# Performance work log

Hardware: AMD Instinct MI355X
Metric: run time of the kernel (lower is better)

## Reference

```python
import jax, jax.numpy as jnp
import numpy as np

E = 304   # embedding size
H = 304   # hidden size
D = 61    # dict_size
B = 256   # batch
T = 512   # frame_num
P = 68    # max_phn_num


def _gru_cell(h, x, Wih, Whh, bih, bhh):
    # PyTorch GRU cell: gates ordered (r, z, n)
    gi = x @ Wih.T + bih            # [B, 3H]
    gh = h @ Whh.T + bhh            # [B, 3H]
    i_r, i_z, i_n = jnp.split(gi, 3, axis=-1)
    h_r, h_z, h_n = jnp.split(gh, 3, axis=-1)
    r = jax.nn.sigmoid(i_r + h_r)
    z = jax.nn.sigmoid(i_z + h_z)
    n = jnp.tanh(i_n + r * h_n)
    return (1.0 - z) * n + z * h


def _run_gru(xs, h0, Wih, Whh, bih, bhh):
    # xs: [B, L, E] -> outputs [B, L, H], final hidden [B, H]
    def step(h, x):
        h = _gru_cell(h, x, Wih, Whh, bih, bhh)
        return h, h
    h_last, outs = jax.lax.scan(step, h0, jnp.swapaxes(xs, 0, 1))
    return jnp.swapaxes(outs, 0, 1), h_last


def setup_inputs() -> dict:
    key = jax.random.key(0)
    ks = jax.random.split(key, 12)
    s = 1.0 / np.sqrt(H)
    u = lambda k, shp: jax.random.uniform(k, shp, jnp.float32, -s, s)
    return {
        'input': jax.random.normal(ks[0], (B, T, E), jnp.float32),
        'target': jax.random.randint(ks[1], (B, P, 1), 0, D),
        'teacher_forcing': 1,
        'enc_Wih': u(ks[2], (3 * H, E)),
        'enc_Whh': u(ks[3], (3 * H, H)),
        'enc_bih': u(ks[4], (3 * H,)),
        'enc_bhh': u(ks[5], (3 * H,)),
        'emb': jax.random.normal(ks[6], (D, E), jnp.float32),
        'dec_Wih': u(ks[7], (3 * H, E)),
        'dec_Whh': u(ks[8], (3 * H, H)),
        'dec_bih': u(ks[9], (3 * H,)),
        'dec_bhh': u(ks[10], (3 * H,)),
        'lin_W': u(ks[11], (D, H)),
        'lin_b': jnp.zeros((D,), jnp.float32),
    }


def reference(input, target, teacher_forcing, enc_Wih, enc_Whh, enc_bih, enc_bhh,
              emb, dec_Wih, dec_Whh, dec_bih, dec_bhh, lin_W, lin_b):
    batch = input.shape[0]
    h0 = jnp.zeros((batch, H), input.dtype)
    # Encoder: the python loop over frames is mathematically a full GRU scan
    enc_outs, enc_h = _run_gru(input, h0, enc_Wih, enc_Whh, enc_bih, enc_bhh)
    # Decoder (teacher_forcing == 1): input tokens are [0, target[:,1], ..., target[:,P-1]]
    toks = jnp.concatenate(
        [jnp.zeros((batch, 1), target.dtype), target[:, 1:, 0]], axis=1)  # [B, P]
    dec_x = emb[toks]                                                      # [B, P, E]
    dec_outs, _ = _run_gru(dec_x, enc_h, dec_Wih, dec_Whh, dec_bih, dec_bhh)
    logits = dec_outs @ lin_W.T + lin_b        # [B, P, D]
    softmaxs = jax.nn.softmax(logits, axis=-1)
    softmax_cal = softmaxs[:, :-1, :].reshape(-1, D)
    target_cal = target[:, 1:, :].reshape(-1)
    asr_outputs = jnp.argmax(softmaxs[:, :-1, :], axis=2)[:, :, None]
    return softmax_cal, target_cal, asr_outputs
```

## Files before the change

### kernel.cpp

```cpp
#include <hip/hip_runtime.h>
#include <math.h>

#define B_   256
#define E_   304
#define H_   304
#define T_   512
#define P_   68
#define PD   67
#define D_   61
#define NCB  16
#define NBG  16
#define RB   16
#define CBH  19
#define GC   57
#define NSTEP (T_ + PD)
#define HW   152
#define BLK_ULL (RB * HW)
#define LROW 328
#define LROWU 164
#define NKS  10
#define RSTR 20
#define SC_LO 2048.0f
#define SC_INV 4.8828125e-4f

typedef unsigned long long ull;
typedef _Float16 half8 __attribute__((ext_vector_type(8)));
typedef _Float16 half2v __attribute__((ext_vector_type(2)));
typedef float f32x4 __attribute__((ext_vector_type(4)));

__global__ __launch_bounds__(256, 1) void gru_persist(
    const float* __restrict__ input,
    const int*   __restrict__ target,
    const float* __restrict__ emb,
    const float* __restrict__ eWih, const float* __restrict__ eWhh,
    const float* __restrict__ ebih, const float* __restrict__ ebhh,
    const float* __restrict__ dWih, const float* __restrict__ dWhh,
    const float* __restrict__ dbih, const float* __restrict__ dbhh,
    float* hbuf,
    float* __restrict__ dec_outs,
    int* flg)
{
    __shared__ _Float16 opH[2][RB * LROW];
    __shared__ _Float16 opL[2][RB * LROW];
    __shared__ float red0[64 * RSTR], red1[64 * RSTR];
    __shared__ float bi_l[2][GC], bh_l[2][GC];

    const int tid  = threadIdx.x;
    const int L    = blockIdx.x;
    const int xcd  = L & 7;
    const int yy   = L >> 3;
    const int cb   = yy & 15;
    const int bg   = ((yy >> 4) << 3) | xcd;
    const int r0   = bg * RB;
    const int c0h  = cb * CBH;
    const int wv   = tid >> 6;
    const int lane = tid & 63;

    half8 wih_h[NKS], wih_l[NKS], whh_h[NKS], whh_l[NKS];

    auto packw = [&](const float* W, half8* wh, half8* wl) {
        int c = wv * 16 + (lane & 15);
        bool valid = (c < GC);
        int g = valid ? c / CBH : 0, j19 = valid ? c - (c / CBH) * CBH : 0;
        const float* wp = W + (size_t)(g * H_ + c0h + j19) * 304;
        int grp = (lane >> 4) * 8;
        #pragma unroll
        for (int ks = 0; ks < NKS; ++ks) {
            half8 vh, vl;
            #pragma unroll
            for (int j = 0; j < 8; ++j) {
                int k = ks * 32 + grp + j;
                float v = (valid && k < 304) ? wp[k] : 0.f;
                _Float16 hi = (_Float16)v;
                float rres = v - (float)hi;
                vh[j] = hi;
                vl[j] = (_Float16)(rres * SC_LO);
            }
            wh[ks] = vh; wl[ks] = vl;
        }
    };

    auto gemm = [&](const _Float16* aH, const _Float16* aL,
                    const half8* wh, const half8* wl, float* red) {
        const int base = (lane & 15) * LROW + (lane >> 4) * 8;
        f32x4 a0 = {0.f, 0.f, 0.f, 0.f}, a1 = a0, a2 = a0;
        #pragma unroll
        for (int ks = 0; ks < NKS; ++ks) {
            half8 Ah = *(const half8*)&aH[base + ks * 32];
            half8 Al = *(const half8*)&aL[base + ks * 32];
            a0 = __builtin_amdgcn_mfma_f32_16x16x32_f16(Ah, wh[ks], a0, 0, 0, 0);
            a1 = __builtin_amdgcn_mfma_f32_16x16x32_f16(Ah, wl[ks], a1, 0, 0, 0);
            a2 = __builtin_amdgcn_mfma_f32_16x16x32_f16(Al, wh[ks], a2, 0, 0, 0);
        }
        f32x4 r = a0 + (a1 + a2) * SC_INV;
        int rb = (wv * 16 + (lane & 15)) * RSTR + (lane >> 4) * 4;
        *(f32x4*)&red[rb] = r;
    };

    auto cvtstore = [&](ull u, int plane, int idx) {
        float a0 = __uint_as_float((unsigned)u);
        float a1 = __uint_as_float((unsigned)(u >> 32));
        _Float16 h0 = (_Float16)a0, h1 = (_Float16)a1;
        float r0f = a0 - (float)h0, r1f = a1 - (float)h1;
        half2v vh; vh.x = h0; vh.y = h1;
        half2v vl; vl.x = (_Float16)(r0f * SC_LO); vl.y = (_Float16)(r1f * SC_LO);
        ((half2v*)&opH[plane][0])[idx] = vh;
        ((half2v*)&opL[plane][0])[idx] = vl;
    };

    packw(eWih, wih_h, wih_l);
    packw(eWhh, whh_h, whh_l);
    if (tid < GC) {
        int g = tid / CBH, j = tid - (tid / CBH) * CBH;
        bi_l[0][tid] = ebih[g * H_ + c0h + j];
        bh_l[0][tid] = ebhh[g * H_ + c0h + j];
        bi_l[1][tid] = dbih[g * H_ + c0h + j];
        bh_l[1][tid] = dbhh[g * H_ + c0h + j];
    }

    for (int f = tid; f < RB * LROW; f += 256) {
        ((unsigned*)opH)[f] = 0u;
        ((unsigned*)opL)[f] = 0u;
    }
    __syncthreads();
    {
        const ull* xin = (const ull*)input;
        #pragma unroll
        for (int i = 0; i < 10; ++i) {
            int f = tid + 256 * i;
            if (i < 9 || f < BLK_ULL) {
                int rr = f / HW, q = f - (f / HW) * HW;
                cvtstore(xin[(size_t)(r0 + rr) * T_ * HW + q], 0, rr * LROWU + q);
            }
        }
    }
    __syncthreads();
    gemm(opH[0], opL[0], wih_h, wih_l, red0);
    ull xr[10];
    {
        const ull* xin = (const ull*)input;
        #pragma unroll
        for (int i = 0; i < 10; ++i) {
            int f = tid + 256 * i;
            if (i < 9 || f < BLK_ULL) {
                int rr = f / HW, q = f - (f / HW) * HW;
                xr[i] = xin[((size_t)(r0 + rr) * T_ + 1) * HW + q];
            }
        }
    }

    for (int s = 0; s < NSTEP; ++s) {
        __syncthreads();
        const bool enc = (s < T_);
        if (s == T_) packw(dWhh, whh_h, whh_l);

        ull hreg[10];
        if (s > 0) {
            const ull* hsrc = (const ull*)(hbuf + (size_t)(s & 1) * (B_ * H_))
                              + (size_t)r0 * HW;
            #pragma unroll
            for (int i = 0; i < 10; ++i) {
                int f = tid + 256 * i;
                if (i < 9 || f < BLK_ULL)
                    hreg[i] = __hip_atomic_load(hsrc + f, __ATOMIC_RELAXED,
                                                __HIP_MEMORY_SCOPE_AGENT);
            }
        }
        if (s + 1 < NSTEP) {
            #pragma unroll
            for (int i = 0; i < 10; ++i) {
                int f = tid + 256 * i;
                if (i < 9 || f < BLK_ULL) {
                    int rr = f / HW, q = f - (f / HW) * HW;
                    cvtstore(xr[i], 0, rr * LROWU + q);
                }
            }
        }
        if (s > 0) {
            #pragma unroll
            for (int i = 0; i < 10; ++i) {
                int f = tid + 256 * i;
                if (i < 9 || f < BLK_ULL) {
                    int rr = f / HW, q = f - (f / HW) * HW;
                    cvtstore(hreg[i], 1, rr * LROWU + q);
                }
            }
        }
        if (s + 2 < NSTEP) {
            if (s + 2 < T_) {
                const ull* xin = (const ull*)input;
                #pragma unroll
                for (int i = 0; i < 10; ++i) {
                    int f = tid + 256 * i;
                    if (i < 9 || f < BLK_ULL) {
                        int rr = f / HW, q = f - (f / HW) * HW;
                        xr[i] = xin[((size_t)(r0 + rr) * T_ + (s + 2)) * HW + q];
                    }
                }
            } else {
                const ull* eb = (const ull*)emb;
                int p2 = s + 2 - T_;
                #pragma unroll
                for (int i = 0; i < 10; ++i) {
                    int f = tid + 256 * i;
                    if (i < 9 || f < BLK_ULL) {
                        int rr = f / HW, q = f - (f / HW) * HW;
                        int tok = (p2 == 0) ? 0 : target[(r0 + rr) * P_ + p2];
                        xr[i] = eb[(size_t)tok * HW + q];
                    }
                }
            }
        }
        __syncthreads();

        gemm(opH[1], opL[1], whh_h, whh_l, red1);
        __syncthreads();

        float* hdst = hbuf + (size_t)((s + 1) & 1) * (B_ * H_);
        for (int o = tid; o < RB * CBH; o += 256) {
            int rr = o / CBH, j = o - (o / CBH) * CBH;
            int col = c0h + j;
            int ph = enc ? 0 : 1;
            float Gi[3], Gh[3];
            #pragma unroll
            for (int g = 0; g < 3; ++g) {
                int c = g * CBH + j;
                Gi[g] = red0[c * RSTR + rr] + bi_l[ph][c];
                Gh[g] = red1[c * RSTR + rr] + bh_l[ph][c];
            }
            float rg = 1.f / (1.f + expf(-(Gi[0] + Gh[0])));
            float zg = 1.f / (1.f + expf(-(Gi[1] + Gh[1])));
            float ng = tanhf(Gi[2] + rg * Gh[2]);
            float hv = (float)opH[1][rr * LROW + col]
                     + (float)opL[1][rr * LROW + col] * SC_INV;
            float hnew = (1.f - zg) * ng + zg * hv;
            __hip_atomic_store(&hdst[(size_t)(r0 + rr) * H_ + col], hnew,
                               __ATOMIC_RELAXED, __HIP_MEMORY_SCOPE_AGENT);
            if (!enc)
                dec_outs[((size_t)(r0 + rr) * PD + (s - T_)) * H_ + col] = hnew;
        }
        __syncthreads();

        if (s + 1 < NSTEP) {
            if (tid == 0)
                __hip_atomic_store(flg + (bg * NCB + cb) * 16, s + 1,
                                   __ATOMIC_RELAXED, __HIP_MEMORY_SCOPE_AGENT);
            if (s + 1 == T_) packw(dWih, wih_h, wih_l);
            gemm(opH[0], opL[0], wih_h, wih_l, red0);
            if (wv == 0) {
                const int tgt = s + 1;
                const int* fp = flg + (bg * NCB + (lane & 15)) * 16;
                for (;;) {
                    int f = (lane < NCB)
                        ? __hip_atomic_load(fp, __ATOMIC_RELAXED,
                                            __HIP_MEMORY_SCOPE_AGENT)
                        : tgt;
                    if (__all(f >= tgt)) break;
                    __builtin_amdgcn_s_sleep(1);
                }
            }
        }
    }
}

__global__ __launch_bounds__(256) void logits_softmax(
    const float* __restrict__ dec_outs,
    const float* __restrict__ linW,
    const float* __restrict__ linb,
    const int* __restrict__ target,
    float* __restrict__ out)
{
    __shared__ float wsm[H_][64];
    __shared__ float rs[4][H_];
    const int tid = threadIdx.x;
    const int wv = tid >> 6, l = tid & 63;

    for (int f = tid; f < H_ * 64; f += 256) {
        int k = f >> 6, ll = f & 63;
        wsm[k][ll] = (ll < D_) ? linW[(size_t)ll * H_ + k] : 0.f;
    }
    const int r = blockIdx.x * 4 + wv;
    const float* rowp = dec_outs + (size_t)r * H_;
    for (int k = l; k < H_; k += 64) rs[wv][k] = rowp[k];
    __syncthreads();

    float acc = -1e30f;
    if (l < D_) {
        acc = linb[l];
        #pragma unroll 4
        for (int k = 0; k < H_; ++k) acc += rs[wv][k] * wsm[k][l];
    }
    float m = acc;
    for (int off = 32; off; off >>= 1) m = fmaxf(m, __shfl_xor(m, off));
    float e = (l < D_) ? expf(acc - m) : 0.f;
    float s = e;
    for (int off = 32; off; off >>= 1) s += __shfl_xor(s, off);
    float av = acc; int ai = l;
    for (int off = 32; off; off >>= 1) {
        float ov = __shfl_xor(av, off);
        int oi = __shfl_xor(ai, off);
        if (ov > av || (ov == av && oi < ai)) { av = ov; ai = oi; }
    }
    const int b = r / PD, p = r - (r / PD) * PD;
    const size_t OFF1 = (size_t)B_ * PD * D_;
    const size_t OFF2 = OFF1 + (size_t)B_ * PD;
    if (l < D_)        out[(size_t)r * D_ + l] = e / s;
    else if (l == D_)  out[OFF1 + r] = (float)target[b * P_ + p + 1];
    else if (l == D_ + 1) out[OFF2 + r] = (float)ai;
}

extern "C" void kernel_launch(void* const* d_in, const int* in_sizes, int n_in,
                              void* d_out, int out_size, void* d_ws, size_t ws_size,
                              hipStream_t stream)
{
    const float* input  = (const float*)d_in[0];
    const int*   target = (const int*)d_in[1];
    const float* eWih = (const float*)d_in[3];
    const float* eWhh = (const float*)d_in[4];
    const float* ebih = (const float*)d_in[5];
    const float* ebhh = (const float*)d_in[6];
    const float* emb  = (const float*)d_in[7];
    const float* dWih = (const float*)d_in[8];
    const float* dWhh = (const float*)d_in[9];
    const float* dbih = (const float*)d_in[10];
    const float* dbhh = (const float*)d_in[11];
    const float* linW = (const float*)d_in[12];
    const float* linb = (const float*)d_in[13];
    float* out = (float*)d_out;

    int*   flg      = (int*)d_ws;
    float* hbuf     = (float*)d_ws + NBG * NCB * 16;
    float* dec_outs = hbuf + 2 * (size_t)B_ * H_;

    (void)hipMemsetAsync(flg, 0, NBG * NCB * 16 * sizeof(int), stream);

    gru_persist<<<dim3(256), 256, 0, stream>>>(
        input, target, emb,
        eWih, eWhh, ebih, ebhh,
        dWih, dWhh, dbih, dbhh,
        hbuf, dec_outs, flg);

    logits_softmax<<<dim3(B_ * PD / 4), 256, 0, stream>>>(
        dec_outs, linW, linb, target, out);
}
```

Measured before the change: 2.390 ms.

## Move flag spin-wait to step start and triple-buffer x operand planes

Moves the cross-block flag wait from the end of each step, where only wave 0 waited, to the start of the next step right before the hidden-state loads. Every wave now polls, and the leading __syncthreads is removed. The x operand is double-buffered across two LDS planes with h in a third, so the next step's input GEMM can write without racing the current staging. The change also swaps expf/tanhf for fast exp and rcp versions, precomputes per-thread index arithmetic, and pads the flag stride to 32 ints. The risks are extra LDS use and slightly less accurate activations, and correctness now depends on every wave seeing the flags before it loads h.

After: 2.444 ms. +2.2%, slower.

```diff
diff --git a/kernel.cpp b/kernel.cpp
--- a/kernel.cpp
+++ b/kernel.cpp
@@ -20,6 +20,7 @@
 #define LROWU 164
 #define NKS  10
 #define RSTR 20
+#define FSTR 32
 #define SC_LO 2048.0f
 #define SC_INV 4.8828125e-4f
 
@@ -27,6 +28,15 @@
 typedef _Float16 half8 __attribute__((ext_vector_type(8)));
 typedef _Float16 half2v __attribute__((ext_vector_type(2)));
 typedef float f32x4 __attribute__((ext_vector_type(4)));
+
+__device__ __forceinline__ float fsigmoid(float x) {
+    float e = __expf(-x);
+    return __builtin_amdgcn_rcpf(1.f + e);
+}
+__device__ __forceinline__ float ftanh(float x) {
+    float e = __expf(2.f * x);
+    return 1.f - 2.f * __builtin_amdgcn_rcpf(1.f + e);
+}
 
 __global__ __launch_bounds__(256, 1) void gru_persist(
     const float* __restrict__ input,
@@ -40,8 +50,8 @@
     float* __restrict__ dec_outs,
     int* flg)
 {
-    __shared__ _Float16 opH[2][RB * LROW];
-    __shared__ _Float16 opL[2][RB * LROW];
+    __shared__ _Float16 opH[3][RB * LROW];
+    __shared__ _Float16 opL[3][RB * LROW];
     __shared__ float red0[64 * RSTR], red1[64 * RSTR];
     __shared__ float bi_l[2][GC], bh_l[2][GC];
 
@@ -57,6 +67,24 @@
     const int lane = tid & 63;
 
     half8 wih_h[NKS], wih_l[NKS], whh_h[NKS], whh_l[NKS];
+
+    int  idxA[10];
+    size_t xbA[10];
+    int  rrA[10], qA[10], tgA[10];
+    #pragma unroll
+    for (int i = 0; i < 10; ++i) {
+        int f = tid + 256 * i;
+        int rr = f / HW, q = f - (f / HW) * HW;
+        rrA[i] = rr; qA[i] = q;
+        idxA[i] = rr * LROWU + q;
+        xbA[i]  = (size_t)(r0 + rr) * T_ * HW + q;
+        tgA[i]  = (r0 + rr) * P_;
+    }
+    const bool gv0 = tid < RB * CBH;
+    const int  gr0 = tid / CBH, gj0 = tid - (tid / CBH) * CBH;
+    const bool gv1 = tid + 256 < RB * CBH;
+    const int  o1  = tid + 256;
+    const int  gr1 = o1 / CBH, gj1 = o1 - (o1 / CBH) * CBH;
 
     auto packw = [&](const float* W, half8* wh, half8* wl) {
         int c = wv * 16 + (lane & 15);
@@ -118,7 +146,7 @@
         bh_l[1][tid] = dbhh[g * H_ + c0h + j];
     }
 
-    for (int f = tid; f < RB * LROW; f += 256) {
+    for (int f = tid; f < (3 * RB * LROW) / 2; f += 256) {
         ((unsigned*)opH)[f] = 0u;
         ((unsigned*)opL)[f] = 0u;
     }
@@ -127,11 +155,8 @@
         const ull* xin = (const ull*)input;
         #pragma unroll
         for (int i = 0; i < 10; ++i) {
-            int f = tid + 256 * i;
-            if (i < 9 || f < BLK_ULL) {
-                int rr = f / HW, q = f - (f / HW) * HW;
-                cvtstore(xin[(size_t)(r0 + rr) * T_ * HW + q], 0, rr * LROWU + q);
-            }
+            if (i < 9 || tid < BLK_ULL - 9 * 256)
+                cvtstore(xin[xbA[i]], 0, idxA[i]);
         }
     }
     __syncthreads();
@@ -141,21 +166,27 @@
         const ull* xin = (const ull*)input;
         #pragma unroll
         for (int i = 0; i < 10; ++i) {
-            int f = tid + 256 * i;
-            if (i < 9 || f < BLK_ULL) {
-                int rr = f / HW, q = f - (f / HW) * HW;
-                xr[i] = xin[((size_t)(r0 + rr) * T_ + 1) * HW + q];
-            }
+            if (i < 9 || tid < BLK_ULL - 9 * 256)
+                xr[i] = xin[xbA[i] + HW];
         }
     }
 
     for (int s = 0; s < NSTEP; ++s) {
-        __syncthreads();
         const bool enc = (s < T_);
         if (s == T_) packw(dWhh, whh_h, whh_l);
 
         ull hreg[10];
         if (s > 0) {
+            const int* fp = flg + (bg * NCB + (lane & 15)) * FSTR;
+            for (;;) {
+                int f = (lane < NCB)
+                    ? __hip_atomic_load(fp, __ATOMIC_RELAXED,
+                                        __HIP_MEMORY_SCOPE_AGENT)
+                    : s;
+                if (__all(f >= s)) break;
+                __builtin_amdgcn_s_sleep(1);
+            }
+            __builtin_amdgcn_sched_barrier(0);
             const ull* hsrc = (const ull*)(hbuf + (size_t)(s & 1) * (B_ * H_))
                               + (size_t)r0 * HW;
             #pragma unroll
@@ -167,60 +198,50 @@
             }
         }
         if (s + 1 < NSTEP) {
+            const int xp = (s + 1) & 1;
             #pragma unroll
             for (int i = 0; i < 10; ++i) {
-                int f = tid + 256 * i;
-                if (i < 9 || f < BLK_ULL) {
-                    int rr = f / HW, q = f - (f / HW) * HW;
-                    cvtstore(xr[i], 0, rr * LROWU + q);
-                }
+                if (i < 9 || tid < BLK_ULL - 9 * 256)
+                    cvtstore(xr[i], xp, idxA[i]);
             }
         }
         if (s > 0) {
             #pragma unroll
             for (int i = 0; i < 10; ++i) {
-                int f = tid + 256 * i;
-                if (i < 9 || f < BLK_ULL) {
-                    int rr = f / HW, q = f - (f / HW) * HW;
-                    cvtstore(hreg[i], 1, rr * LROWU + q);
-                }
+                if (i < 9 || tid < BLK_ULL - 9 * 256)
+                    cvtstore(hreg[i], 2, idxA[i]);
             }
         }
         if (s + 2 < NSTEP) {
             if (s + 2 < T_) {
                 const ull* xin = (const ull*)input;
+                const size_t off = (size_t)(s + 2) * HW;
                 #pragma unroll
                 for (int i = 0; i < 10; ++i) {
-                    int f = tid + 256 * i;
-                    if (i < 9 || f < BLK_ULL) {
-                        int rr = f / HW, q = f - (f / HW) * HW;
-                        xr[i] = xin[((size_t)(r0 + rr) * T_ + (s + 2)) * HW + q];
-                    }
+                    if (i < 9 || tid < BLK_ULL - 9 * 256)
+                        xr[i] = xin[xbA[i] + off];
                 }
             } else {
                 const ull* eb = (const ull*)emb;
                 int p2 = s + 2 - T_;
                 #pragma unroll
                 for (int i = 0; i < 10; ++i) {
-                    int f = tid + 256 * i;
-                    if (i < 9 || f < BLK_ULL) {
-                        int rr = f / HW, q = f - (f / HW) * HW;
-                        int tok = (p2 == 0) ? 0 : target[(r0 + rr) * P_ + p2];
-                        xr[i] = eb[(size_t)tok * HW + q];
+                    if (i < 9 || tid < BLK_ULL - 9 * 256) {
+                        int tok = (p2 == 0) ? 0 : target[tgA[i] + p2];
+                        xr[i] = eb[(size_t)tok * HW + qA[i]];
                     }
                 }
             }
         }
         __syncthreads();
 
-        gemm(opH[1], opL[1], whh_h, whh_l, red1);
+        gemm(opH[2], opL[2], whh_h, whh_l, red1);
         __syncthreads();
 
         float* hdst = hbuf + (size_t)((s + 1) & 1) * (B_ * H_);
-        for (int o = tid; o < RB * CBH; o += 256) {
-            int rr = o / CBH, j = o - (o / CBH) * CBH;
+        const int ph = enc ? 0 : 1;
+        auto gate_one = [&](int rr, int j) {
             int col = c0h + j;
-            int ph = enc ? 0 : 1;
             float Gi[3], Gh[3];
             #pragma unroll
             for (int g = 0; g < 3; ++g) {
@@ -228,37 +249,27 @@
                 Gi[g] = red0[c * RSTR + rr] + bi_l[ph][c];
                 Gh[g] = red1[c * RSTR + rr] + bh_l[ph][c];
             }
-            float rg = 1.f / (1.f + expf(-(Gi[0] + Gh[0])));
-            float zg = 1.f / (1.f + expf(-(Gi[1] + Gh[1])));
-            float ng = tanhf(Gi[2] + rg * Gh[2]);
-            float hv = (float)opH[1][rr * LROW + col]
-                     + (float)opL[1][rr * LROW + col] * SC_INV;
+            float rg = fsigmoid(Gi[0] + Gh[0]);
+            float zg = fsigmoid(Gi[1] + Gh[1]);
+            float ng = ftanh(Gi[2] + rg * Gh[2]);
+            float hv = (float)opH[2][rr * LROW + col]
+                     + (float)opL[2][rr * LROW + col] * SC_INV;
             float hnew = (1.f - zg) * ng + zg * hv;
             __hip_atomic_store(&hdst[(size_t)(r0 + rr) * H_ + col], hnew,
                                __ATOMIC_RELAXED, __HIP_MEMORY_SCOPE_AGENT);
             if (!enc)
                 dec_outs[((size_t)(r0 + rr) * PD + (s - T_)) * H_ + col] = hnew;
-        }
+        };
+        if (gv0) gate_one(gr0, gj0);
+        if (gv1) gate_one(gr1, gj1);
         __syncthreads();
 
         if (s + 1 < NSTEP) {
             if (tid == 0)
-                __hip_atomic_store(flg + (bg * NCB + cb) * 16, s + 1,
+                __hip_atomic_store(flg + (bg * NCB + cb) * FSTR, s + 1,
                                    __ATOMIC_RELAXED, __HIP_MEMORY_SCOPE_AGENT);
             if (s + 1 == T_) packw(dWih, wih_h, wih_l);
-            gemm(opH[0], opL[0], wih_h, wih_l, red0);
-            if (wv == 0) {
-                const int tgt = s + 1;
-                const int* fp = flg + (bg * NCB + (lane & 15)) * 16;
-                for (;;) {
-                    int f = (lane < NCB)
-                        ? __hip_atomic_load(fp, __ATOMIC_RELAXED,
-                                            __HIP_MEMORY_SCOPE_AGENT)
-                        : tgt;
-                    if (__all(f >= tgt)) break;
-                    __builtin_amdgcn_s_sleep(1);
-                }
-            }
+            gemm(opH[(s + 1) & 1], opL[(s + 1) & 1], wih_h, wih_l, red0);
         }
     }
 }
@@ -329,10 +340,10 @@
     float* out = (float*)d_out;
 
     int*   flg      = (int*)d_ws;
-    float* hbuf     = (float*)d_ws + NBG * NCB * 16;
+    float* hbuf     = (float*)d_ws + NBG * NCB * FSTR;
     float* dec_outs = hbuf + 2 * (size_t)B_ * H_;
 
-    (void)hipMemsetAsync(flg, 0, NBG * NCB * 16 * sizeof(int), stream);
+    (void)hipMemsetAsync(flg, 0, NBG * NCB * FSTR * sizeof(int), stream);
 
     gru_persist<<<dim3(256), 256, 0, stream>>>(
         input, target, emb,
```
